# Kernel optimization log

Hardware: AMD Instinct MI355X
Metric: run time of the kernel (lower is better)

## Reference

```python
import jax, jax.numpy as jnp
import numpy as np
import math

B, S, HID = 2, 2048, 1024
NH = 16
HD = HID // NH          # 64
VD = HD // 2            # 32 value dim
TD = HD - VD            # 32 type dim
EPS = 1e-6


def setup_inputs() -> dict:
    key = jax.random.key(0)
    ks = jax.random.split(key, 12)
    std = 1.0 / math.sqrt(HID)
    xav = math.sqrt(6.0 / (TD + TD))
    return {
        "x": jax.random.normal(ks[0], (B, S, HID), dtype=jnp.float32),
        "q_w": jax.random.uniform(ks[1], (HID, HID), jnp.float32, -std, std),
        "q_b": jax.random.uniform(ks[2], (HID,), jnp.float32, -std, std),
        "k_w": jax.random.uniform(ks[3], (HID, HID), jnp.float32, -std, std),
        "k_b": jax.random.uniform(ks[4], (HID,), jnp.float32, -std, std),
        "v_w": jax.random.uniform(ks[5], (HID, HID), jnp.float32, -std, std),
        "v_b": jax.random.uniform(ks[6], (HID,), jnp.float32, -std, std),
        "out_w": jax.random.uniform(ks[7], (HID, HID), jnp.float32, -std, std),
        "out_b": jax.random.uniform(ks[8], (HID,), jnp.float32, -std, std),
        "type_bilinear": jax.random.uniform(ks[9], (NH, TD, TD), jnp.float32, -xav, xav),
        "type_bias": jnp.full((NH,), 2.0, dtype=jnp.float32),
        "mask": jnp.ones((B, S), dtype=jnp.int32),
    }


def reference(x, q_w, q_b, k_w, k_b, v_w, v_b, out_w, out_b, type_bilinear, type_bias, mask):
    # projections: [B,S,HID] -> [B,NH,S,HD]
    def proj(w, b):
        y = jnp.einsum("bsi,io->bso", x, w) + b
        return y.reshape(B, S, NH, HD).transpose(0, 2, 1, 3)

    q = proj(q_w, q_b)
    k = proj(k_w, k_b)
    v = proj(v_w, v_b)

    q_val, q_type = q[..., :VD], q[..., VD:]
    k_val, k_type = k[..., :VD], k[..., VD:]

    # standard value score: [B,NH,S,S]
    val_scores = jnp.einsum("bhqd,bhkd->bhqk", q_val, k_val) / math.sqrt(VD)

    # per-head bilinear type score: q_type @ W_h @ k_type^T + bias_h
    qt = jnp.einsum("bhqd,hde->bhqe", q_type, type_bilinear)
    type_scores = jnp.einsum("bhqe,bhke->bhqk", qt, k_type) + type_bias[None, :, None, None]
    type_unif = jax.nn.sigmoid(type_scores)

    scores = val_scores + jnp.log(type_unif + EPS)

    # mask: [B,S] -> broadcast over heads and query dim (keys masked)
    m = (mask[:, None, None, :] != 0)
    scores = jnp.where(m, scores, -jnp.inf)

    attn = jax.nn.softmax(scores, axis=-1)
    out = jnp.einsum("bhqk,bhkd->bhqd", attn, v)          # [B,NH,S,HD]
    out = out.transpose(0, 2, 1, 3).reshape(B, S, HID)
    return jnp.einsum("bsi,io->bso", out, out_w) + out_b
```

## Files before the change

kernel.cpp:

```cpp
#include <hip/hip_runtime.h>
#include <hip/hip_bf16.h>
#include <math.h>

typedef __attribute__((ext_vector_type(8))) short bf16x8;
typedef __attribute__((ext_vector_type(4))) float f32x4;
typedef __attribute__((ext_vector_type(4))) int   i32x4;

#define NHh 16
#define Sq  2048
#define HIDq 1024
#define HDq 64
#define LOG2E 1.4426950408889634f

#if __has_builtin(__builtin_amdgcn_exp2f)
#define EXP2F(x) __builtin_amdgcn_exp2f(x)
#else
#define EXP2F(x) exp2f(x)
#endif
#if __has_builtin(__builtin_amdgcn_rcpf)
#define RCPF(x) __builtin_amdgcn_rcpf(x)
#else
#define RCPF(x) (1.0f/(x))
#endif

__device__ __forceinline__ unsigned short f2bf(float f){
  union { float f; unsigned u; } v; v.f = f;
  unsigned r = v.u + 0x7fffu + ((v.u >> 16) & 1u);
  return (unsigned short)(r >> 16);
}
__device__ __forceinline__ float bf2f(unsigned short s){
  union { unsigned u; float f; } v; v.u = ((unsigned)s) << 16;
  return v.f;
}
__device__ __forceinline__ unsigned pk2bf(float lo, float hi){
  union { __hip_bfloat162 h; unsigned u; } w;
  w.h = __float22bfloat162_rn(make_float2(lo, hi));
  return w.u;
}

__device__ __forceinline__ void gload_lds16(const unsigned short* g, unsigned short* l){
  __builtin_amdgcn_global_load_lds(
      (const __attribute__((address_space(1))) unsigned int*)g,
      (__attribute__((address_space(3))) unsigned int*)l, 16, 0, 0);
}

__global__ __launch_bounds__(256) void convert_x(const float* __restrict__ in,
                                                 unsigned short* __restrict__ out, int n8){
  int i = blockIdx.x*256 + threadIdx.x;
  if (i >= n8) return;
  const f32x4* p = (const f32x4*)(in + (size_t)i*8);
  f32x4 a = p[0], b = p[1];
  union { unsigned short us[8]; i32x4 v; } o;
  #pragma unroll
  for (int j=0;j<4;j++){ o.us[j] = f2bf(a[j]); o.us[4+j] = f2bf(b[j]); }
  *(i32x4*)(out + (size_t)i*8) = o.v;
}

__global__ __launch_bounds__(256) void transpose_w(const float* __restrict__ w0, const float* __restrict__ w1,
                                                   const float* __restrict__ w2, const float* __restrict__ w3,
                                                   unsigned short* __restrict__ wT){
  __shared__ float tile[32][33];
  int z = blockIdx.z;
  const float* w = (z==0)?w0:(z==1)?w1:(z==2)?w2:w3;
  unsigned short* dst = wT + (size_t)z*HIDq*HIDq;
  int tx = threadIdx.x, ty = threadIdx.y;
  int n0 = blockIdx.x*32, k0 = blockIdx.y*32;
  #pragma unroll
  for (int i=ty;i<32;i+=8) tile[i][tx] = w[(size_t)(k0+i)*HIDq + n0+tx];
  __syncthreads();
  #pragma unroll
  for (int i=ty;i<32;i+=8) dst[(size_t)(n0+i)*HIDq + k0+tx] = f2bf(tile[tx][i]);
}

__device__ __forceinline__ void gemm_core_gl(const unsigned short* __restrict__ Ag,
                                             const unsigned short* __restrict__ Bg,
                                             unsigned short* As, unsigned short* Bs,
                                             int t, int wv, int lane, int wr, int wc, int lr, int g,
                                             f32x4 acc[4][4]){
  for (int k0=0; k0<HIDq; k0+=64){
    __syncthreads();
    #pragma unroll
    for (int j=0;j<4;j++){
      int flat = (j*4+wv)*64 + lane;
      int row = flat>>3, c8 = (flat&7)*8;
      gload_lds16(Ag + (size_t)row*HIDq + k0 + c8, &As[flat*8]);
      gload_lds16(Bg + (size_t)row*HIDq + k0 + c8, &Bs[flat*8]);
    }
    __syncthreads();
    #pragma unroll
    for (int ks=0; ks<2; ks++){
      bf16x8 af[4], bfv[4];
      #pragma unroll
      for (int m=0;m<4;m++) af[m]  = *(bf16x8*)&As[(wr+m*16+lr)*64 + ks*32 + g*8];
      #pragma unroll
      for (int n=0;n<4;n++) bfv[n] = *(bf16x8*)&Bs[(wc+n*16+lr)*64 + ks*32 + g*8];
      #pragma unroll
      for (int n=0;n<4;n++)
        #pragma unroll
        for (int m=0;m<4;m++)
          acc[n][m] = __builtin_amdgcn_mfma_f32_16x16x32_bf16(bfv[n], af[m], acc[n][m], 0,0,0);
    }
  }
}

__global__ __launch_bounds__(256) void gemm_qkv(const unsigned short* __restrict__ xbf,
    const unsigned short* __restrict__ wT,
    const float* __restrict__ q_b, const float* __restrict__ k_b, const float* __restrict__ v_b,
    unsigned short* __restrict__ Qeff, unsigned short* __restrict__ Keff,
    unsigned short* __restrict__ Vt){
  __shared__ unsigned short As[128*64];
  __shared__ unsigned short Bs[128*64];
  const int t = threadIdx.x;
  const int wv = t>>6, lane = t&63, g = lane>>4, lr = lane&15;
  const int wr = (wv>>1)*64, wc = (wv&1)*64;
  f32x4 acc[4][4] = {};
  int id = blockIdx.y*gridDim.x + blockIdx.x;
  int cpx = (gridDim.x*gridDim.y) >> 3;
  int sid = (id&7)*cpx + (id>>3);
  const int xb = sid % gridDim.x, yb = sid / gridDim.x;
  const float VS = 0.25501335f;

  if (xb < 16){
    const int row0 = yb*128, col0 = xb*128;
    gemm_core_gl(xbf + (size_t)row0*HIDq, wT + (size_t)col0*HIDq, As, Bs, t, wv, lane, wr, wc, lr, g, acc);
    #pragma unroll
    for (int n=0;n<4;n++){
      #pragma unroll
      for (int m=0;m<4;m++){
        int row = row0 + wr + m*16 + lr;
        int b_ = row>>11, ss = row&2047;
        int colb = col0 + wc + n*16 + g*4;
        int seg = colb>>10, cw = colb&1023;
        int hh = cw>>6, d = cw&63;
        const float* bp = seg ? k_b : q_b;
        f32x4 bb = *(const f32x4*)&bp[cw];
        float sc = seg ? 1.0f : (d < 32 ? VS : -LOG2E);
        unsigned short* E = seg ? Keff : Qeff;
        float v0 = (acc[n][m][0]+bb[0])*sc, v1 = (acc[n][m][1]+bb[1])*sc;
        float v2 = (acc[n][m][2]+bb[2])*sc, v3 = (acc[n][m][3]+bb[3])*sc;
        union { unsigned u[2]; unsigned long long ll; } W;
        W.u[0] = pk2bf(v0,v1); W.u[1] = pk2bf(v2,v3);
        *(unsigned long long*)&E[(((size_t)b_*NHh+hh)*Sq+ss)*HDq + d] = W.ll;
      }
    }
  } else {
    const int row0 = (xb-16)*128, col0 = yb*128;
    gemm_core_gl(wT + (size_t)2*HIDq*HIDq + (size_t)row0*HIDq, xbf + (size_t)col0*HIDq,
                 As, Bs, t, wv, lane, wr, wc, lr, g, acc);
    #pragma unroll
    for (int n=0;n<4;n++){
      #pragma unroll
      for (int m=0;m<4;m++){
        int chan = row0 + wr + m*16 + lr;
        int hh = chan>>6, d = chan&63;
        float bv = v_b[chan];
        int colb = col0 + wc + n*16 + g*4;
        int b_ = colb>>11, ss = colb&2047;
        union { unsigned u[2]; unsigned long long ll; } W;
        W.u[0] = pk2bf(acc[n][m][0]+bv, acc[n][m][1]+bv);
        W.u[1] = pk2bf(acc[n][m][2]+bv, acc[n][m][3]+bv);
        *(unsigned long long*)&Vt[(((size_t)b_*NHh+hh)*HDq + d)*Sq + ss] = W.ll;
      }
    }
  }
}

__global__ __launch_bounds__(256) void gemm_out(const unsigned short* __restrict__ A,
                                                const unsigned short* __restrict__ Bt,
                                                const float* __restrict__ bias,
                                                float* __restrict__ C){
  __shared__ unsigned short As[128*64];
  __shared__ unsigned short Bs[128*64];
  const int t = threadIdx.x;
  const int wv = t>>6, lane = t&63, g = lane>>4, lr = lane&15;
  const int wr = (wv>>1)*64, wc = (wv&1)*64;
  int id = blockIdx.y*gridDim.x + blockIdx.x;
  int cpx = (gridDim.x*gridDim.y) >> 3;
  int sid = (id&7)*cpx + (id>>3);
  const int xb = sid % gridDim.x, yb = sid / gridDim.x;
  const int row0 = yb*128, col0 = xb*128;
  f32x4 acc[4][4] = {};
  gemm_core_gl(A + (size_t)row0*HIDq, Bt + (size_t)col0*HIDq, As, Bs, t, wv, lane, wr, wc, lr, g, acc);
  #pragma unroll
  for (int n=0;n<4;n++){
    #pragma unroll
    for (int m=0;m<4;m++){
      int row = row0 + wr + m*16 + lr;
      int colb = col0 + wc + n*16 + g*4;
      f32x4 bb = *(const f32x4*)&bias[colb];
      f32x4 o = acc[n][m] + bb;
      *(f32x4*)&C[(size_t)row*HIDq + colb] = o;
    }
  }
}

__global__ __launch_bounds__(512,2) void attn_kernel(
    const unsigned short* __restrict__ Qe, const unsigned short* __restrict__ Ke,
    const unsigned short* __restrict__ Vt, const float* __restrict__ Tb,
    const float* __restrict__ tbias, const int* __restrict__ mask,
    unsigned short* __restrict__ Obuf)
{
  __shared__ __align__(16) unsigned char smem[49664];
  unsigned short* Ks = (unsigned short*)smem;
  unsigned short* Vs = (unsigned short*)(smem + 16384);
  unsigned short* Pl = (unsigned short*)(smem + 32768);
  float* mskf = (float*)(smem + 49152);
  float* qls = (float*)smem;
  unsigned short* qtls = Pl;

  const int t = threadIdx.x;
  const int dd = blockIdx.x;
  const int slot = dd>>3, xcd = dd&7;
  const int x = slot & 15;
  const int bh = ((slot>>4)<<3) | xcd;
  const int h = bh & 15, b = bh >> 4;
  const int q0 = x*128;
  const int wv = t>>6, lane = t&63, g = lane>>4, lr = lane&15;

  const unsigned short* Qb  = Qe + (((size_t)b*NHh+h)*Sq + q0)*HDq;
  const unsigned short* Kb  = Ke + ((size_t)b*NHh+h)*(size_t)Sq*HDq;
  const unsigned short* Vtb = Vt + ((size_t)b*NHh+h)*(size_t)HDq*Sq;
  const int* Mb = mask + (size_t)b*Sq;

  i32x4 kreg[2], vreg[2];
  #pragma unroll
  for (int i=0;i<2;i++){
    int c = t + i*512;
    int kr = c>>3, kc = (c&7)*8;
    kreg[i] = *(const i32x4*)(Kb + (size_t)kr*HDq + kc);
    int vd = c>>4, vc = (c&15)*8;
    vreg[i] = *(const i32x4*)(Vtb + (size_t)vd*Sq + vc);
  }
  int mv = (t<128) ? Mb[t] : 0;

  {
    int row = t>>2, c8 = (t&3)*8;
    bf16x8 v = *(const bf16x8*)(Qb + (size_t)row*HDq + 32 + c8);
    #pragma unroll
    for (int j=0;j<8;j++) qls[row*33 + c8 + j] = bf2f((unsigned short)v[j]);
  }
  __syncthreads();
  {
    int row = t&127, e0 = (t>>7)*8;
    const float* Th = Tb + (size_t)h*1024;
    float a[8] = {};
    #pragma unroll 4
    for (int d=0; d<32; d++){
      float qd = qls[row*33 + d];
      const f32x4* tp = (const f32x4*)(Th + d*32 + e0);
      f32x4 t0 = tp[0], t1 = tp[1];
      a[0]+=qd*t0[0]; a[1]+=qd*t0[1]; a[2]+=qd*t0[2]; a[3]+=qd*t0[3];
      a[4]+=qd*t1[0]; a[5]+=qd*t1[1]; a[6]+=qd*t1[2]; a[7]+=qd*t1[3];
    }
    union { unsigned u[2]; unsigned long long ll; } W0, W1;
    W0.u[0]=pk2bf(a[0],a[1]); W0.u[1]=pk2bf(a[2],a[3]);
    W1.u[0]=pk2bf(a[4],a[5]); W1.u[1]=pk2bf(a[6],a[7]);
    *(unsigned long long*)&qtls[row*40 + e0]     = W0.ll;
    *(unsigned long long*)&qtls[row*40 + e0 + 4] = W1.ll;
  }
  bf16x8 qvf = *(const bf16x8*)(Qb + (size_t)(wv*16+lr)*HDq + g*8);
  __syncthreads();
  bf16x8 qtn = *(const bf16x8*)&qtls[(wv*16+lr)*40 + g*8];

  const float tbn = -tbias[h]*LOG2E;
  const f32x4 tbc = {tbn,tbn,tbn,tbn};
  f32x4 oT[4] = {};
  f32x4 lsum = {0.f,0.f,0.f,0.f};
  unsigned short* Pw = &Pl[wv*1024 + lr*64];
  const int swp = (lr&7)*8;
  bf16x8 onesf;
  #pragma unroll
  for (int j=0;j<8;j++) onesf[j] = (short)0x3F80;

  for (int kt=0; kt<Sq; kt+=128){
    __syncthreads();
    #pragma unroll
    for (int i=0;i<2;i++){
      int c = t + i*512;
      int kr = c>>3, kc = (c&7)*8;
      *(i32x4*)&Ks[kr*64 + (kc ^ ((kr&7)*8))] = kreg[i];
      int vd = c>>4, vc = (c&15)*8;
      *(i32x4*)&Vs[vd*128 + (vc ^ ((vd&15)*8))] = vreg[i];
    }
    if (t<128) mskf[t] = mv ? 0.f : -1e30f;
    __syncthreads();
    if (kt + 128 < Sq){
      #pragma unroll
      for (int i=0;i<2;i++){
        int c = t + i*512;
        int kr = c>>3, kc = (c&7)*8;
        kreg[i] = *(const i32x4*)(Kb + (size_t)(kt+128+kr)*HDq + kc);
        int vd = c>>4, vc = (c&15)*8;
        vreg[i] = *(const i32x4*)(Vtb + (size_t)vd*Sq + kt + 128 + vc);
      }
      if (t<128) mv = Mb[kt+128+t];
    }

    #pragma unroll
    for (int kh=0; kh<2; kh++){
      f32x4 sv[4], st[4];
      __builtin_amdgcn_s_setprio(1);
      #pragma unroll
      for (int ks=0; ks<4; ks++){
        int krow = kh*64 + ks*16 + lr;
        const unsigned short* kb = &Ks[krow*64];
        int sw = (krow&7)*8;
        bf16x8 kf0 = *(const bf16x8*)(kb + ((g*8) ^ sw));
        bf16x8 kf1 = *(const bf16x8*)(kb + ((32 + g*8) ^ sw));
        f32x4 madd = *(const f32x4*)&mskf[kh*64 + ks*16 + g*4];
        sv[ks] = __builtin_amdgcn_mfma_f32_16x16x32_bf16(kf0, qvf, madd, 0,0,0);
        st[ks] = __builtin_amdgcn_mfma_f32_16x16x32_bf16(kf1, qtn, tbc, 0,0,0);
      }
      __builtin_amdgcn_s_setprio(0);
      #pragma unroll
      for (int ks=0; ks<4; ks++){
        float p0 = EXP2F(sv[ks][0]) * RCPF(1.f + EXP2F(st[ks][0]));
        float p1 = EXP2F(sv[ks][1]) * RCPF(1.f + EXP2F(st[ks][1]));
        float p2 = EXP2F(sv[ks][2]) * RCPF(1.f + EXP2F(st[ks][2]));
        float p3 = EXP2F(sv[ks][3]) * RCPF(1.f + EXP2F(st[ks][3]));
        union { unsigned u[2]; unsigned long long ll; } W;
        W.u[0] = pk2bf(p0,p1); W.u[1] = pk2bf(p2,p3);
        *(unsigned long long*)(Pw + ((ks*16 + g*4) ^ swp)) = W.ll;
      }
      #pragma unroll
      for (int ks2=0; ks2<2; ks2++){
        bf16x8 pf = *(const bf16x8*)(Pw + ((ks2*32 + g*8) ^ swp));
        __builtin_amdgcn_s_setprio(1);
        lsum = __builtin_amdgcn_mfma_f32_16x16x32_bf16(onesf, pf, lsum, 0,0,0);
        #pragma unroll
        for (int db=0; db<4; db++){
          int vrow = db*16 + lr;
          bf16x8 vf = *(const bf16x8*)(&Vs[vrow*128] + ((kh*64 + ks2*32 + g*8) ^ ((vrow&15)*8)));
          oT[db] = __builtin_amdgcn_mfma_f32_16x16x32_bf16(vf, pf, oT[db], 0,0,0);
        }
        __builtin_amdgcn_s_setprio(0);
      }
    }
  }

  float linv = (lsum[0] > 0.f) ? RCPF(lsum[0]) : 0.f;
  int srow = q0 + wv*16 + lr;
  unsigned short* Ob = Obuf + ((size_t)b*Sq + srow)*HIDq + h*HDq;
  #pragma unroll
  for (int db=0; db<4; db++){
    union { unsigned u[2]; unsigned long long ll; } W;
    W.u[0] = pk2bf(oT[db][0]*linv, oT[db][1]*linv);
    W.u[1] = pk2bf(oT[db][2]*linv, oT[db][3]*linv);
    *(unsigned long long*)(Ob + db*16 + g*4) = W.ll;
  }
}

extern "C" void kernel_launch(void* const* d_in, const int* in_sizes, int n_in,
                              void* d_out, int out_size, void* d_ws, size_t ws_size,
                              hipStream_t stream) {
  const float* x     = (const float*)d_in[0];
  const float* q_w   = (const float*)d_in[1];
  const float* q_b   = (const float*)d_in[2];
  const float* k_w   = (const float*)d_in[3];
  const float* k_b   = (const float*)d_in[4];
  const float* v_w   = (const float*)d_in[5];
  const float* v_b   = (const float*)d_in[6];
  const float* out_w = (const float*)d_in[7];
  const float* out_b = (const float*)d_in[8];
  const float* Tb    = (const float*)d_in[9];
  const float* tbias = (const float*)d_in[10];
  const int*   mask  = (const int*)d_in[11];

  const size_t MROWS = 4096;
  unsigned short* xbf  = (unsigned short*)d_ws;
  unsigned short* wT   = xbf  + MROWS*HIDq;
  unsigned short* Qeff = wT   + (size_t)4*HIDq*HIDq;
  unsigned short* Keff = Qeff + MROWS*HIDq;
  unsigned short* Vt   = Keff + MROWS*HIDq;
  unsigned short* Obuf = Vt   + MROWS*HIDq;

  convert_x<<<dim3((int)(MROWS*HIDq/8/256)), dim3(256), 0, stream>>>(x, xbf, (int)(MROWS*HIDq/8));
  transpose_w<<<dim3(32,32,4), dim3(32,8), 0, stream>>>(q_w, k_w, v_w, out_w, wT);

  gemm_qkv<<<dim3(24,32), dim3(256), 0, stream>>>(xbf, wT, q_b, k_b, v_b, Qeff, Keff, Vt);

  attn_kernel<<<dim3(512), dim3(512), 0, stream>>>(Qeff, Keff, Vt, Tb, tbias, mask, Obuf);

  gemm_out<<<dim3(8,32), dim3(256), 0, stream>>>(Obuf, wT + (size_t)3*HIDq*HIDq, out_b, (float*)d_out);
}
```

Measured before the change: 173.7 us.

## Double-buffer attention K/V via direct LDS loads, precompute mask, simplify GEMM core

The attention kernel now double-buffers K/V tiles in LDS using direct global-to-LDS loads with swizzled addresses, replacing the old register-staged prefetch. The additive mask is precomputed into a float buffer by extra blocks of convert_x and read straight from global memory. The GEMM core switches to K-step 32, register-staged loads into padded LDS (stride 40), and drops the block-ID remapping. LDS use in the attention kernel grows to 80KB, which with launch_bounds(512,2) may limit occupancy. The simpler GEMM path and the lost L2-friendly block ordering may also cost speed.

After: 170.9 us. No clear change (-1.6%).

```diff
diff --git a/kernel.cpp b/kernel.cpp
--- a/kernel.cpp
+++ b/kernel.cpp
@@ -45,8 +45,18 @@
 }
 
 __global__ __launch_bounds__(256) void convert_x(const float* __restrict__ in,
-                                                 unsigned short* __restrict__ out, int n8){
-  int i = blockIdx.x*256 + threadIdx.x;
+                                                 unsigned short* __restrict__ out, int n8,
+                                                 const int* __restrict__ mask,
+                                                 float* __restrict__ Mf){
+  int bid = blockIdx.x;
+  int nmain = gridDim.x - 2;
+  if (bid >= nmain){
+    int base = (bid - nmain)*2048 + threadIdx.x*8;
+    #pragma unroll
+    for (int j=0;j<8;j++) Mf[base+j] = mask[base+j] ? 0.f : -1e30f;
+    return;
+  }
+  int i = bid*256 + threadIdx.x;
   if (i >= n8) return;
   const f32x4* p = (const f32x4*)(in + (size_t)i*8);
   f32x4 a = p[0], b = p[1];
@@ -72,34 +82,31 @@
   for (int i=ty;i<32;i+=8) dst[(size_t)(n0+i)*HIDq + k0+tx] = f2bf(tile[tx][i]);
 }
 
-__device__ __forceinline__ void gemm_core_gl(const unsigned short* __restrict__ Ag,
-                                             const unsigned short* __restrict__ Bg,
-                                             unsigned short* As, unsigned short* Bs,
-                                             int t, int wv, int lane, int wr, int wc, int lr, int g,
-                                             f32x4 acc[4][4]){
-  for (int k0=0; k0<HIDq; k0+=64){
+__device__ __forceinline__ void gemm_core(const unsigned short* __restrict__ Ag,
+                                          const unsigned short* __restrict__ Bg,
+                                          unsigned short* As, unsigned short* Bs,
+                                          int t, int wr, int wc, int lr, int g,
+                                          f32x4 acc[4][4]){
+  for (int k0=0; k0<HIDq; k0+=32){
     __syncthreads();
     #pragma unroll
-    for (int j=0;j<4;j++){
-      int flat = (j*4+wv)*64 + lane;
-      int row = flat>>3, c8 = (flat&7)*8;
-      gload_lds16(Ag + (size_t)row*HIDq + k0 + c8, &As[flat*8]);
-      gload_lds16(Bg + (size_t)row*HIDq + k0 + c8, &Bs[flat*8]);
+    for (int i=0;i<2;i++){
+      int flat = t + i*256;
+      int row = flat>>2, kc = (flat&3)*8;
+      *(i32x4*)&As[row*40+kc] = *(const i32x4*)(Ag + (size_t)row*HIDq + k0 + kc);
+      *(i32x4*)&Bs[row*40+kc] = *(const i32x4*)(Bg + (size_t)row*HIDq + k0 + kc);
     }
     __syncthreads();
-    #pragma unroll
-    for (int ks=0; ks<2; ks++){
-      bf16x8 af[4], bfv[4];
-      #pragma unroll
-      for (int m=0;m<4;m++) af[m]  = *(bf16x8*)&As[(wr+m*16+lr)*64 + ks*32 + g*8];
-      #pragma unroll
-      for (int n=0;n<4;n++) bfv[n] = *(bf16x8*)&Bs[(wc+n*16+lr)*64 + ks*32 + g*8];
-      #pragma unroll
-      for (int n=0;n<4;n++)
-        #pragma unroll
-        for (int m=0;m<4;m++)
-          acc[n][m] = __builtin_amdgcn_mfma_f32_16x16x32_bf16(bfv[n], af[m], acc[n][m], 0,0,0);
-    }
+    bf16x8 af[4], bfv[4];
+    #pragma unroll
+    for (int m=0;m<4;m++) af[m]  = *(bf16x8*)&As[(wr+m*16+lr)*40 + g*8];
+    #pragma unroll
+    for (int n=0;n<4;n++) bfv[n] = *(bf16x8*)&Bs[(wc+n*16+lr)*40 + g*8];
+    #pragma unroll
+    for (int n=0;n<4;n++)
+      #pragma unroll
+      for (int m=0;m<4;m++)
+        acc[n][m] = __builtin_amdgcn_mfma_f32_16x16x32_bf16(bfv[n], af[m], acc[n][m], 0,0,0);
   }
 }
 
@@ -108,21 +115,18 @@
     const float* __restrict__ q_b, const float* __restrict__ k_b, const float* __restrict__ v_b,
     unsigned short* __restrict__ Qeff, unsigned short* __restrict__ Keff,
     unsigned short* __restrict__ Vt){
-  __shared__ unsigned short As[128*64];
-  __shared__ unsigned short Bs[128*64];
+  __shared__ unsigned short As[128*40];
+  __shared__ unsigned short Bs[128*40];
   const int t = threadIdx.x;
   const int wv = t>>6, lane = t&63, g = lane>>4, lr = lane&15;
   const int wr = (wv>>1)*64, wc = (wv&1)*64;
   f32x4 acc[4][4] = {};
-  int id = blockIdx.y*gridDim.x + blockIdx.x;
-  int cpx = (gridDim.x*gridDim.y) >> 3;
-  int sid = (id&7)*cpx + (id>>3);
-  const int xb = sid % gridDim.x, yb = sid / gridDim.x;
+  const int xb = blockIdx.x, yb = blockIdx.y;
   const float VS = 0.25501335f;
 
   if (xb < 16){
     const int row0 = yb*128, col0 = xb*128;
-    gemm_core_gl(xbf + (size_t)row0*HIDq, wT + (size_t)col0*HIDq, As, Bs, t, wv, lane, wr, wc, lr, g, acc);
+    gemm_core(xbf + (size_t)row0*HIDq, wT + (size_t)col0*HIDq, As, Bs, t, wr, wc, lr, g, acc);
     #pragma unroll
     for (int n=0;n<4;n++){
       #pragma unroll
@@ -145,8 +149,8 @@
     }
   } else {
     const int row0 = (xb-16)*128, col0 = yb*128;
-    gemm_core_gl(wT + (size_t)2*HIDq*HIDq + (size_t)row0*HIDq, xbf + (size_t)col0*HIDq,
-                 As, Bs, t, wv, lane, wr, wc, lr, g, acc);
+    gemm_core(wT + (size_t)2*HIDq*HIDq + (size_t)row0*HIDq, xbf + (size_t)col0*HIDq,
+              As, Bs, t, wr, wc, lr, g, acc);
     #pragma unroll
     for (int n=0;n<4;n++){
       #pragma unroll
@@ -169,18 +173,14 @@
                                                 const unsigned short* __restrict__ Bt,
                                                 const float* __restrict__ bias,
                                                 float* __restrict__ C){
-  __shared__ unsigned short As[128*64];
-  __shared__ unsigned short Bs[128*64];
+  __shared__ unsigned short As[128*40];
+  __shared__ unsigned short Bs[128*40];
   const int t = threadIdx.x;
   const int wv = t>>6, lane = t&63, g = lane>>4, lr = lane&15;
   const int wr = (wv>>1)*64, wc = (wv&1)*64;
-  int id = blockIdx.y*gridDim.x + blockIdx.x;
-  int cpx = (gridDim.x*gridDim.y) >> 3;
-  int sid = (id&7)*cpx + (id>>3);
-  const int xb = sid % gridDim.x, yb = sid / gridDim.x;
-  const int row0 = yb*128, col0 = xb*128;
+  const int row0 = blockIdx.y*128, col0 = blockIdx.x*128;
   f32x4 acc[4][4] = {};
-  gemm_core_gl(A + (size_t)row0*HIDq, Bt + (size_t)col0*HIDq, As, Bs, t, wv, lane, wr, wc, lr, g, acc);
+  gemm_core(A + (size_t)row0*HIDq, Bt + (size_t)col0*HIDq, As, Bs, t, wr, wc, lr, g, acc);
   #pragma unroll
   for (int n=0;n<4;n++){
     #pragma unroll
@@ -197,15 +197,16 @@
 __global__ __launch_bounds__(512,2) void attn_kernel(
     const unsigned short* __restrict__ Qe, const unsigned short* __restrict__ Ke,
     const unsigned short* __restrict__ Vt, const float* __restrict__ Tb,
-    const float* __restrict__ tbias, const int* __restrict__ mask,
+    const float* __restrict__ tbias, const float* __restrict__ Mf,
     unsigned short* __restrict__ Obuf)
 {
-  __shared__ __align__(16) unsigned char smem[49664];
-  unsigned short* Ks = (unsigned short*)smem;
-  unsigned short* Vs = (unsigned short*)(smem + 16384);
-  unsigned short* Pl = (unsigned short*)(smem + 32768);
-  float* mskf = (float*)(smem + 49152);
-  float* qls = (float*)smem;
+  __shared__ __align__(16) unsigned char smem[81920];
+  unsigned short* Ks0 = (unsigned short*)smem;
+  unsigned short* Vs0 = (unsigned short*)(smem + 16384);
+  unsigned short* Ks1 = (unsigned short*)(smem + 32768);
+  unsigned short* Vs1 = (unsigned short*)(smem + 49152);
+  unsigned short* Pl  = (unsigned short*)(smem + 65536);
+  float* qls = (float*)(smem + 32768);
   unsigned short* qtls = Pl;
 
   const int t = threadIdx.x;
@@ -220,18 +221,18 @@
   const unsigned short* Qb  = Qe + (((size_t)b*NHh+h)*Sq + q0)*HDq;
   const unsigned short* Kb  = Ke + ((size_t)b*NHh+h)*(size_t)Sq*HDq;
   const unsigned short* Vtb = Vt + ((size_t)b*NHh+h)*(size_t)HDq*Sq;
-  const int* Mb = mask + (size_t)b*Sq;
-
-  i32x4 kreg[2], vreg[2];
-  #pragma unroll
-  for (int i=0;i<2;i++){
-    int c = t + i*512;
-    int kr = c>>3, kc = (c&7)*8;
-    kreg[i] = *(const i32x4*)(Kb + (size_t)kr*HDq + kc);
-    int vd = c>>4, vc = (c&15)*8;
-    vreg[i] = *(const i32x4*)(Vtb + (size_t)vd*Sq + vc);
-  }
-  int mv = (t<128) ? Mb[t] : 0;
+  const float* Mfb = Mf + (size_t)b*Sq;
+
+  const int ch0 = (wv*2+0)*64 + lane, ch1 = (wv*2+1)*64 + lane;
+
+  {
+    int kr0 = ch0>>3, kc0 = ch0&7, kr1 = ch1>>3, kc1 = ch1&7;
+    gload_lds16(Kb + (size_t)kr0*HDq + (kc0 ^ (kr0&7))*8, Ks0 + ch0*8);
+    gload_lds16(Kb + (size_t)kr1*HDq + (kc1 ^ (kr1&7))*8, Ks0 + ch1*8);
+    int vd0 = ch0>>4, vc0 = ch0&15, vd1 = ch1>>4, vc1 = ch1&15;
+    gload_lds16(Vtb + (size_t)vd0*Sq + (vc0 ^ (vd0&15))*8, Vs0 + ch0*8);
+    gload_lds16(Vtb + (size_t)vd1*Sq + (vc1 ^ (vd1&15))*8, Vs0 + ch1*8);
+  }
 
   {
     int row = t>>2, c8 = (t&3)*8;
@@ -252,6 +253,7 @@
       a[0]+=qd*t0[0]; a[1]+=qd*t0[1]; a[2]+=qd*t0[2]; a[3]+=qd*t0[3];
       a[4]+=qd*t1[0]; a[5]+=qd*t1[1]; a[6]+=qd*t1[2]; a[7]+=qd*t1[3];
     }
+    __syncthreads();
     union { unsigned u[2]; unsigned long long ll; } W0, W1;
     W0.u[0]=pk2bf(a[0],a[1]); W0.u[1]=pk2bf(a[2],a[3]);
     W1.u[0]=pk2bf(a[4],a[5]); W1.u[1]=pk2bf(a[6],a[7]);
@@ -261,6 +263,7 @@
   bf16x8 qvf = *(const bf16x8*)(Qb + (size_t)(wv*16+lr)*HDq + g*8);
   __syncthreads();
   bf16x8 qtn = *(const bf16x8*)&qtls[(wv*16+lr)*40 + g*8];
+  __syncthreads();
 
   const float tbn = -tbias[h]*LOG2E;
   const f32x4 tbc = {tbn,tbn,tbn,tbn};
@@ -272,28 +275,23 @@
   #pragma unroll
   for (int j=0;j<8;j++) onesf[j] = (short)0x3F80;
 
+  unsigned short *Kc = Ks0, *Vc = Vs0, *Kn = Ks1, *Vn = Vs1;
+
   for (int kt=0; kt<Sq; kt+=128){
-    __syncthreads();
-    #pragma unroll
-    for (int i=0;i<2;i++){
-      int c = t + i*512;
-      int kr = c>>3, kc = (c&7)*8;
-      *(i32x4*)&Ks[kr*64 + (kc ^ ((kr&7)*8))] = kreg[i];
-      int vd = c>>4, vc = (c&15)*8;
-      *(i32x4*)&Vs[vd*128 + (vc ^ ((vd&15)*8))] = vreg[i];
-    }
-    if (t<128) mskf[t] = mv ? 0.f : -1e30f;
-    __syncthreads();
+    f32x4 madd[2][4];
+    #pragma unroll
+    for (int kh2=0; kh2<2; kh2++)
+      #pragma unroll
+      for (int ks=0; ks<4; ks++)
+        madd[kh2][ks] = *(const f32x4*)(Mfb + kt + kh2*64 + ks*16 + g*4);
     if (kt + 128 < Sq){
-      #pragma unroll
-      for (int i=0;i<2;i++){
-        int c = t + i*512;
-        int kr = c>>3, kc = (c&7)*8;
-        kreg[i] = *(const i32x4*)(Kb + (size_t)(kt+128+kr)*HDq + kc);
-        int vd = c>>4, vc = (c&15)*8;
-        vreg[i] = *(const i32x4*)(Vtb + (size_t)vd*Sq + kt + 128 + vc);
-      }
-      if (t<128) mv = Mb[kt+128+t];
+      int kt2 = kt + 128;
+      int kr0 = ch0>>3, kc0 = ch0&7, kr1 = ch1>>3, kc1 = ch1&7;
+      gload_lds16(Kb + (size_t)(kt2+kr0)*HDq + (kc0 ^ (kr0&7))*8, Kn + ch0*8);
+      gload_lds16(Kb + (size_t)(kt2+kr1)*HDq + (kc1 ^ (kr1&7))*8, Kn + ch1*8);
+      int vd0 = ch0>>4, vc0 = ch0&15, vd1 = ch1>>4, vc1 = ch1&15;
+      gload_lds16(Vtb + (size_t)vd0*Sq + kt2 + (vc0 ^ (vd0&15))*8, Vn + ch0*8);
+      gload_lds16(Vtb + (size_t)vd1*Sq + kt2 + (vc1 ^ (vd1&15))*8, Vn + ch1*8);
     }
 
     #pragma unroll
@@ -303,12 +301,11 @@
       #pragma unroll
       for (int ks=0; ks<4; ks++){
         int krow = kh*64 + ks*16 + lr;
-        const unsigned short* kb = &Ks[krow*64];
+        const unsigned short* kb = &Kc[krow*64];
         int sw = (krow&7)*8;
         bf16x8 kf0 = *(const bf16x8*)(kb + ((g*8) ^ sw));
         bf16x8 kf1 = *(const bf16x8*)(kb + ((32 + g*8) ^ sw));
-        f32x4 madd = *(const f32x4*)&mskf[kh*64 + ks*16 + g*4];
-        sv[ks] = __builtin_amdgcn_mfma_f32_16x16x32_bf16(kf0, qvf, madd, 0,0,0);
+        sv[ks] = __builtin_amdgcn_mfma_f32_16x16x32_bf16(kf0, qvf, madd[kh][ks], 0,0,0);
         st[ks] = __builtin_amdgcn_mfma_f32_16x16x32_bf16(kf1, qtn, tbc, 0,0,0);
       }
       __builtin_amdgcn_s_setprio(0);
@@ -330,12 +327,16 @@
         #pragma unroll
         for (int db=0; db<4; db++){
           int vrow = db*16 + lr;
-          bf16x8 vf = *(const bf16x8*)(&Vs[vrow*128] + ((kh*64 + ks2*32 + g*8) ^ ((vrow&15)*8)));
+          bf16x8 vf = *(const bf16x8*)(&Vc[vrow*128] + ((kh*64 + ks2*32 + g*8) ^ ((vrow&15)*8)));
           oT[db] = __builtin_amdgcn_mfma_f32_16x16x32_bf16(vf, pf, oT[db], 0,0,0);
         }
         __builtin_amdgcn_s_setprio(0);
       }
     }
+    __syncthreads();
+    unsigned short* tp;
+    tp = Kc; Kc = Kn; Kn = tp;
+    tp = Vc; Vc = Vn; Vn = tp;
   }
 
   float linv = (lsum[0] > 0.f) ? RCPF(lsum[0]) : 0.f;
@@ -373,13 +374,15 @@
   unsigned short* Keff = Qeff + MROWS*HIDq;
   unsigned short* Vt   = Keff + MROWS*HIDq;
   unsigned short* Obuf = Vt   + MROWS*HIDq;
-
-  convert_x<<<dim3((int)(MROWS*HIDq/8/256)), dim3(256), 0, stream>>>(x, xbf, (int)(MROWS*HIDq/8));
+  float*          Mf   = (float*)(Obuf + MROWS*HIDq);
+
+  int n8 = (int)(MROWS*HIDq/8);
+  convert_x<<<dim3(n8/256 + 2), dim3(256), 0, stream>>>(x, xbf, n8, mask, Mf);
   transpose_w<<<dim3(32,32,4), dim3(32,8), 0, stream>>>(q_w, k_w, v_w, out_w, wT);
 
   gemm_qkv<<<dim3(24,32), dim3(256), 0, stream>>>(xbf, wT, q_b, k_b, v_b, Qeff, Keff, Vt);
 
-  attn_kernel<<<dim3(512), dim3(512), 0, stream>>>(Qeff, Keff, Vt, Tb, tbias, mask, Obuf);
+  attn_kernel<<<dim3(512), dim3(512), 0, stream>>>(Qeff, Keff, Vt, Tb, tbias, Mf, Obuf);
 
   gemm_out<<<dim3(8,32), dim3(256), 0, stream>>>(Obuf, wT + (size_t)3*HIDq*HIDq, out_b, (float*)d_out);
 }
```
